# Kernel tuning notes

Hardware: AMD Instinct MI355X
Metric: run time of the kernel (lower is better)

The kernel has to match this reference:

```python
import jax, jax.numpy as jnp
import numpy as np

THRESH = 0.1
BN_EPS = 1e-5
B, N, C_IN, C_HID, C_OUT = 4096, 128, 64, 256, 128


def setup_inputs() -> dict:
    key = jax.random.key(0)
    ks = jax.random.split(key, 10)
    a = jax.random.uniform(ks[0], (B, N, N), dtype=jnp.float32)
    v = jax.random.normal(ks[1], (B, N, C_IN), dtype=jnp.float32)
    # MLP params: Linear(C_IN->C_HID) + BN + ReLU + Linear(C_HID->C_OUT) + BN + ReLU
    W1 = jax.random.normal(ks[2], (C_IN, C_HID), dtype=jnp.float32) / np.sqrt(C_IN)
    b1 = jnp.zeros((C_HID,), jnp.float32)
    g1 = 1.0 + 0.1 * jax.random.normal(ks[3], (C_HID,), dtype=jnp.float32)
    be1 = 0.1 * jax.random.normal(ks[4], (C_HID,), dtype=jnp.float32)
    rm1 = 0.1 * jax.random.normal(ks[5], (C_HID,), dtype=jnp.float32)
    rv1 = jnp.ones((C_HID,), jnp.float32)
    W2 = jax.random.normal(ks[6], (C_HID, C_OUT), dtype=jnp.float32) / np.sqrt(C_HID)
    b2 = jnp.zeros((C_OUT,), jnp.float32)
    g2 = 1.0 + 0.1 * jax.random.normal(ks[7], (C_OUT,), dtype=jnp.float32)
    be2 = 0.1 * jax.random.normal(ks[8], (C_OUT,), dtype=jnp.float32)
    rm2 = 0.1 * jax.random.normal(ks[9], (C_OUT,), dtype=jnp.float32)
    rv2 = jnp.ones((C_OUT,), jnp.float32)
    return {"a": a, "v": v, "W1": W1, "b1": b1, "g1": g1, "be1": be1, "rm1": rm1, "rv1": rv1,
            "W2": W2, "b2": b2, "g2": g2, "be2": be2, "rm2": rm2, "rv2": rv2}


def reference(a, v, W1, b1, g1, be1, rm1, rv1, W2, b2, g2, be2, rm2, rv2):
    # threshold adjacency
    a_th = (a >= THRESH).astype(v.dtype)            # [B, N, N]
    # D^-0.5 A D^-0.5 as row/col rescaling (equivalent to diag_embed + bmm)
    d_inv_sqrt = jnp.sum(a_th, axis=-1) ** -0.5     # [B, N]
    a_bar = d_inv_sqrt[:, :, None] * a_th * d_inv_sqrt[:, None, :]
    # propagate
    h = jnp.einsum('bnm,bmc->bnc', a_bar, v)        # [B, N, C_IN]
    x = h.reshape(-1, h.shape[-1])                  # [(B N), C_IN]
    # MLP with BatchNorm in eval mode (running stats), dropout is identity in eval
    x = x @ W1 + b1
    x = (x - rm1) * jax.lax.rsqrt(rv1 + BN_EPS) * g1 + be1
    x = jax.nn.relu(x)
    x = x @ W2 + b2
    x = (x - rm2) * jax.lax.rsqrt(rv2 + BN_EPS) * g2 + be2
    x = jax.nn.relu(x)
    return x
```

## Files before the change

kernel.cpp:

```cpp
#include <hip/hip_runtime.h>


#define THRESH 0.1f
#define BN_EPS 1e-5f

typedef __attribute__((ext_vector_type(8))) short bf16x8;
typedef __attribute__((ext_vector_type(4))) float f32x4;

__device__ __forceinline__ unsigned short f2bf(float f) {
    union { float f; unsigned u; } x; x.f = f;
    unsigned r = x.u + 0x7FFFu + ((x.u >> 16) & 1u);
    return (unsigned short)(r >> 16);
}

__device__ __forceinline__ unsigned cvt_pk(float lo, float hi) {
    unsigned r;
    asm("v_cvt_pk_bf16_f32 %0, %1, %2" : "=v"(r) : "v"(lo), "v"(hi));
    return r;
}

__global__ void gcn_prep(const float* __restrict__ W1, const float* __restrict__ b1,
                         const float* __restrict__ g1, const float* __restrict__ be1,
                         const float* __restrict__ rm1, const float* __restrict__ rv1,
                         const float* __restrict__ W2, const float* __restrict__ b2,
                         const float* __restrict__ g2, const float* __restrict__ be2,
                         const float* __restrict__ rm2, const float* __restrict__ rv2,
                         unsigned short* __restrict__ W1s, unsigned short* __restrict__ W2s,
                         float* __restrict__ sh1, float* __restrict__ sh2) {
    int t = blockIdx.x * blockDim.x + threadIdx.x;
    if (t < 256 * 64) {
        int n = t >> 6, kp = t & 63;
        int sp = kp >> 3, lo = kp & 7;
        int s  = sp ^ (n & 7);
        int k2 = s * 8 + lo;
        int r = k2 & 3, aa = (k2 >> 2) & 1, gg = (k2 >> 3) & 3, T = k2 >> 5;
        int k = T * 32 + aa * 16 + gg * 4 + r;
        float sc = g1[n] * rsqrtf(rv1[n] + BN_EPS);
        W1s[t] = f2bf(W1[k * 256 + n] * sc);
    }
    {
        int n = t >> 8, kp = t & 255;
        int sp = kp >> 3, lo = kp & 7;
        int s  = sp ^ (n & 7);
        int k2 = s * 8 + lo;
        int r = k2 & 3, aa = (k2 >> 2) & 1, gg = (k2 >> 3) & 3, T = k2 >> 5;
        int k = T * 32 + aa * 16 + gg * 4 + r;
        float sc = g2[n] * rsqrtf(rv2[n] + BN_EPS);
        W2s[t] = f2bf(W2[k * 128 + n] * sc);
    }
    if (t < 256) {
        float s = g1[t] * rsqrtf(rv1[t] + BN_EPS);
        sh1[t] = (b1[t] - rm1[t]) * s + be1[t];
    }
    if (t < 128) {
        float s = g2[t] * rsqrtf(rv2[t] + BN_EPS);
        sh2[t] = (b2[t] - rm2[t]) * s + be2[t];
    }
}

__global__ void __launch_bounds__(512, 1)
gcn_fused(const float* __restrict__ A, const float* __restrict__ V,
          const unsigned short* __restrict__ W1s, const unsigned short* __restrict__ W2s,
          const float* __restrict__ sh1g, const float* __restrict__ sh2g,
          float* __restrict__ out) {
    __shared__ char smem[134656];
    unsigned short* W1L = (unsigned short*)smem;
    unsigned short* W2L = (unsigned short*)(smem + 32768);
    float* s_sh1 = (float*)(smem + 133120);
    float* s_sh2 = (float*)(smem + 134144);

    const int t    = threadIdx.x;
    const int lane = t & 63;
    const int w    = t >> 6;
    const int r16  = lane & 15;
    const int g    = lane >> 4;
    const int bs   = w >> 2;
    const int wl   = w & 3;

    unsigned short* vt = (unsigned short*)(smem + 98304) + bs * (64 * 136);

#pragma unroll
    for (int q = 0; q < 4; ++q)
        *(f32x4*)(smem + t * 64 + q * 16) = *(const f32x4*)((const char*)W1s + t * 64 + q * 16);
#pragma unroll
    for (int q = 0; q < 8; ++q)
        *(f32x4*)(smem + 32768 + t * 128 + q * 16) =
            *(const f32x4*)((const char*)W2s + t * 128 + q * 16);
    if (t < 256) s_sh1[t] = sh1g[t];
    if (t < 128) s_sh2[t] = sh2g[t];

    const size_t b00 = (size_t)blockIdx.x * 16;

    const int mloc  = lane & 31;
    const int chalf = (lane >> 5) * 32;

    bf16x8 afrag[2][4];
    float dinv0, dinv1;
    {
        const size_t b = b00 + bs;
        const float* vb = V + b * 8192 + (size_t)(32 * wl + mloc) * 64 + chalf;
        f32x4 pv[8];
#pragma unroll
        for (int q = 0; q < 8; ++q) pv[q] = *(const f32x4*)(vb + 4 * q);

        const float* ab = A + b * 16384 + (size_t)(32 * wl + r16) * 128;
        int cnt0 = 0, cnt1 = 0;
#pragma unroll
        for (int mt = 0; mt < 2; ++mt)
#pragma unroll
            for (int ks = 0; ks < 4; ++ks) {
                const float* p = ab + mt * 2048 + ks * 32 + 8 * g;
                f32x4 x0 = *(const f32x4*)p;
                f32x4 x1 = *(const f32x4*)(p + 4);
                union { unsigned short s[8]; bf16x8 v; } u;
                u.s[0] = (x0.x >= THRESH) ? (unsigned short)0x3F80u : (unsigned short)0u;
                u.s[1] = (x0.y >= THRESH) ? (unsigned short)0x3F80u : (unsigned short)0u;
                u.s[2] = (x0.z >= THRESH) ? (unsigned short)0x3F80u : (unsigned short)0u;
                u.s[3] = (x0.w >= THRESH) ? (unsigned short)0x3F80u : (unsigned short)0u;
                u.s[4] = (x1.x >= THRESH) ? (unsigned short)0x3F80u : (unsigned short)0u;
                u.s[5] = (x1.y >= THRESH) ? (unsigned short)0x3F80u : (unsigned short)0u;
                u.s[6] = (x1.z >= THRESH) ? (unsigned short)0x3F80u : (unsigned short)0u;
                u.s[7] = (x1.w >= THRESH) ? (unsigned short)0x3F80u : (unsigned short)0u;
                afrag[mt][ks] = u.v;
                int c = (x0.x >= THRESH) + (x0.y >= THRESH) + (x0.z >= THRESH) + (x0.w >= THRESH)
                      + (x1.x >= THRESH) + (x1.y >= THRESH) + (x1.z >= THRESH) + (x1.w >= THRESH);
                if (mt == 0) cnt0 += c; else cnt1 += c;
            }
        cnt0 += __shfl_xor(cnt0, 16); cnt0 += __shfl_xor(cnt0, 32);
        cnt1 += __shfl_xor(cnt1, 16); cnt1 += __shfl_xor(cnt1, 32);
        dinv0 = rsqrtf((float)cnt0);
        dinv1 = rsqrtf((float)cnt1);

        float dm = (lane & 16) ? dinv1 : dinv0;
        int m = 32 * wl + mloc;
#pragma unroll
        for (int q = 0; q < 8; ++q) {
            int c = chalf + 4 * q;
            vt[(c + 0) * 136 + m] = f2bf(pv[q].x * dm);
            vt[(c + 1) * 136 + m] = f2bf(pv[q].y * dm);
            vt[(c + 2) * 136 + m] = f2bf(pv[q].z * dm);
            vt[(c + 3) * 136 + m] = f2bf(pv[q].w * dm);
        }
    }
    __syncthreads();

#pragma unroll 1
    for (int it = 0; it < 8; ++it) {
        const size_t b  = b00 + it * 2 + bs;
        const size_t mb = (size_t)(32 * wl);

        f32x4 acc1[4][2];
#pragma unroll
        for (int ct = 0; ct < 4; ++ct)
#pragma unroll
            for (int mt = 0; mt < 2; ++mt) acc1[ct][mt] = f32x4{0.f, 0.f, 0.f, 0.f};
#pragma unroll
        for (int ks = 0; ks < 4; ++ks)
#pragma unroll
            for (int ct = 0; ct < 4; ++ct) {
                bf16x8 av = *(const bf16x8*)(vt + (ct * 16 + r16) * 136 + ks * 32 + 8 * g);
                acc1[ct][0] = __builtin_amdgcn_mfma_f32_16x16x32_bf16(av, afrag[0][ks], acc1[ct][0], 0, 0, 0);
                acc1[ct][1] = __builtin_amdgcn_mfma_f32_16x16x32_bf16(av, afrag[1][ks], acc1[ct][1], 0, 0, 0);
            }
        bf16x8 bh[2][2];
#pragma unroll
        for (int mt = 0; mt < 2; ++mt) {
            float d = (mt == 0) ? dinv0 : dinv1;
#pragma unroll
            for (int ks2 = 0; ks2 < 2; ++ks2) {
                union { unsigned u[4]; bf16x8 v; } pk;
                pk.u[0] = cvt_pk(acc1[2 * ks2][mt][0] * d,     acc1[2 * ks2][mt][1] * d);
                pk.u[1] = cvt_pk(acc1[2 * ks2][mt][2] * d,     acc1[2 * ks2][mt][3] * d);
                pk.u[2] = cvt_pk(acc1[2 * ks2 + 1][mt][0] * d, acc1[2 * ks2 + 1][mt][1] * d);
                pk.u[3] = cvt_pk(acc1[2 * ks2 + 1][mt][2] * d, acc1[2 * ks2 + 1][mt][3] * d);
                bh[mt][ks2] = pk.v;
            }
        }
        __syncthreads();

        f32x4 acc3[2][8];
#pragma unroll
        for (int mt = 0; mt < 2; ++mt)
#pragma unroll
            for (int ct = 0; ct < 8; ++ct) acc3[mt][ct] = f32x4{0.f, 0.f, 0.f, 0.f};

#pragma unroll
        for (int T = 0; T < 8; ++T) {
            f32x4 a2[2][2];
#pragma unroll
            for (int mt = 0; mt < 2; ++mt)
#pragma unroll
                for (int ctp = 0; ctp < 2; ++ctp) a2[mt][ctp] = f32x4{0.f, 0.f, 0.f, 0.f};
#pragma unroll
            for (int ctp = 0; ctp < 2; ++ctp) {
                int n = (2 * T + ctp) * 16 + r16;
#pragma unroll
                for (int ks2 = 0; ks2 < 2; ++ks2) {
                    int sp = (ks2 * 4 + g) ^ (n & 7);
                    bf16x8 aw = *(const bf16x8*)(W1L + n * 64 + sp * 8);
                    a2[0][ctp] = __builtin_amdgcn_mfma_f32_16x16x32_bf16(aw, bh[0][ks2], a2[0][ctp], 0, 0, 0);
                    a2[1][ctp] = __builtin_amdgcn_mfma_f32_16x16x32_bf16(aw, bh[1][ks2], a2[1][ctp], 0, 0, 0);
                }
            }
            union { unsigned u[4]; bf16x8 v; } af[2];
#pragma unroll
            for (int ctp = 0; ctp < 2; ++ctp) {
                f32x4 sh = *(const f32x4*)(s_sh1 + (2 * T + ctp) * 16 + 4 * g);
#pragma unroll
                for (int mt = 0; mt < 2; ++mt) {
                    float y0 = fmaxf(a2[mt][ctp][0] + sh.x, 0.f);
                    float y1 = fmaxf(a2[mt][ctp][1] + sh.y, 0.f);
                    float y2 = fmaxf(a2[mt][ctp][2] + sh.z, 0.f);
                    float y3 = fmaxf(a2[mt][ctp][3] + sh.w, 0.f);
                    af[mt].u[2 * ctp + 0] = cvt_pk(y0, y1);
                    af[mt].u[2 * ctp + 1] = cvt_pk(y2, y3);
                }
            }
#pragma unroll
            for (int ct3 = 0; ct3 < 8; ++ct3) {
                int n  = ct3 * 16 + r16;
                int sp = (T * 4 + g) ^ (n & 7);
                bf16x8 bw = *(const bf16x8*)(W2L + n * 256 + sp * 8);
                acc3[0][ct3] = __builtin_amdgcn_mfma_f32_16x16x32_bf16(af[0].v, bw, acc3[0][ct3], 0, 0, 0);
                acc3[1][ct3] = __builtin_amdgcn_mfma_f32_16x16x32_bf16(af[1].v, bw, acc3[1][ct3], 0, 0, 0);
            }
        }

        float* ob = out + (b * 128 + mb) * 128;
#pragma unroll
        for (int ct3 = 0; ct3 < 8; ++ct3) {
            int c = ct3 * 16 + r16;
            float sh = s_sh2[c];
#pragma unroll
            for (int mt = 0; mt < 2; ++mt)
#pragma unroll
                for (int r = 0; r < 4; ++r) {
                    int row = 16 * mt + 4 * g + r;
                    ob[row * 128 + c] = fmaxf(acc3[mt][ct3][r] + sh, 0.f);
                }
        }

        if (it < 7) {
            const size_t bn = b00 + (it + 1) * 2 + bs;
            const float* vb = V + bn * 8192 + (size_t)(32 * wl + mloc) * 64 + chalf;
            f32x4 pv[8];
#pragma unroll
            for (int q = 0; q < 8; ++q) pv[q] = *(const f32x4*)(vb + 4 * q);

            const float* ab = A + bn * 16384 + (size_t)(32 * wl + r16) * 128;
            int cnt0 = 0, cnt1 = 0;
#pragma unroll
            for (int mt = 0; mt < 2; ++mt)
#pragma unroll
                for (int ks = 0; ks < 4; ++ks) {
                    const float* p = ab + mt * 2048 + ks * 32 + 8 * g;
                    f32x4 x0 = *(const f32x4*)p;
                    f32x4 x1 = *(const f32x4*)(p + 4);
                    union { unsigned short s[8]; bf16x8 v; } u;
                    u.s[0] = (x0.x >= THRESH) ? (unsigned short)0x3F80u : (unsigned short)0u;
                    u.s[1] = (x0.y >= THRESH) ? (unsigned short)0x3F80u : (unsigned short)0u;
                    u.s[2] = (x0.z >= THRESH) ? (unsigned short)0x3F80u : (unsigned short)0u;
                    u.s[3] = (x0.w >= THRESH) ? (unsigned short)0x3F80u : (unsigned short)0u;
                    u.s[4] = (x1.x >= THRESH) ? (unsigned short)0x3F80u : (unsigned short)0u;
                    u.s[5] = (x1.y >= THRESH) ? (unsigned short)0x3F80u : (unsigned short)0u;
                    u.s[6] = (x1.z >= THRESH) ? (unsigned short)0x3F80u : (unsigned short)0u;
                    u.s[7] = (x1.w >= THRESH) ? (unsigned short)0x3F80u : (unsigned short)0u;
                    afrag[mt][ks] = u.v;
                    int c = (x0.x >= THRESH) + (x0.y >= THRESH) + (x0.z >= THRESH) + (x0.w >= THRESH)
                          + (x1.x >= THRESH) + (x1.y >= THRESH) + (x1.z >= THRESH) + (x1.w >= THRESH);
                    if (mt == 0) cnt0 += c; else cnt1 += c;
                }
            cnt0 += __shfl_xor(cnt0, 16); cnt0 += __shfl_xor(cnt0, 32);
            cnt1 += __shfl_xor(cnt1, 16); cnt1 += __shfl_xor(cnt1, 32);
            dinv0 = rsqrtf((float)cnt0);
            dinv1 = rsqrtf((float)cnt1);

            float dm = (lane & 16) ? dinv1 : dinv0;
            int m = 32 * wl + mloc;
#pragma unroll
            for (int q = 0; q < 8; ++q) {
                int c = chalf + 4 * q;
                vt[(c + 0) * 136 + m] = f2bf(pv[q].x * dm);
                vt[(c + 1) * 136 + m] = f2bf(pv[q].y * dm);
                vt[(c + 2) * 136 + m] = f2bf(pv[q].z * dm);
                vt[(c + 3) * 136 + m] = f2bf(pv[q].w * dm);
            }
            __syncthreads();
        }
    }
}

extern "C" void kernel_launch(void* const* d_in, const int* in_sizes, int n_in,
                              void* d_out, int out_size, void* d_ws, size_t ws_size,
                              hipStream_t stream) {
    (void)in_sizes; (void)n_in; (void)out_size; (void)ws_size;
    const float* a   = (const float*)d_in[0];
    const float* v   = (const float*)d_in[1];
    const float* W1  = (const float*)d_in[2];
    const float* b1  = (const float*)d_in[3];
    const float* g1  = (const float*)d_in[4];
    const float* be1 = (const float*)d_in[5];
    const float* rm1 = (const float*)d_in[6];
    const float* rv1 = (const float*)d_in[7];
    const float* W2  = (const float*)d_in[8];
    const float* b2  = (const float*)d_in[9];
    const float* g2  = (const float*)d_in[10];
    const float* be2 = (const float*)d_in[11];
    const float* rm2 = (const float*)d_in[12];
    const float* rv2 = (const float*)d_in[13];

    char* ws = (char*)d_ws;
    unsigned short* W1s = (unsigned short*)ws;
    unsigned short* W2s = (unsigned short*)(ws + 32768);
    float* sh1 = (float*)(ws + 98304);
    float* sh2 = (float*)(ws + 99328);

    gcn_prep<<<128, 256, 0, stream>>>(W1, b1, g1, be1, rm1, rv1,
                                      W2, b2, g2, be2, rm2, rv2,
                                      W1s, W2s, sh1, sh2);
    gcn_fused<<<256, 512, 0, stream>>>(a, v, W1s, W2s, sh1, sh2, (float*)d_out);
}
```

Measured before the change: 189.5 us.

## Prefetch next batch's adjacency and features during MLP, pack threshold masks as bits

Global loads of the next batch's V and A tiles are now issued before the second MLP GEMM. The A thresholding is interleaved across the T loop, so memory latency overlaps MFMA work instead of sitting in a serialized tail. Adjacency fragments are kept as 32-bit bitmasks, with degrees counted by popcount, and expanded to bf16 fragments only when needed, which reduces register pressure. On the last iteration each block still performs a clamped, redundant prefetch and a vt write, adding some extra memory traffic.

New measurement: 217.0 us. 1.15x slower.

```diff
diff --git a/kernel.cpp b/kernel.cpp
--- a/kernel.cpp
+++ b/kernel.cpp
@@ -17,6 +17,26 @@
     unsigned r;
     asm("v_cvt_pk_bf16_f32 %0, %1, %2" : "=v"(r) : "v"(lo), "v"(hi));
     return r;
+}
+
+__device__ __forceinline__ unsigned thbyte(f32x4 x0, f32x4 x1) {
+    return  (unsigned)(x0.x >= THRESH)
+         | ((unsigned)(x0.y >= THRESH) << 1)
+         | ((unsigned)(x0.z >= THRESH) << 2)
+         | ((unsigned)(x0.w >= THRESH) << 3)
+         | ((unsigned)(x1.x >= THRESH) << 4)
+         | ((unsigned)(x1.y >= THRESH) << 5)
+         | ((unsigned)(x1.z >= THRESH) << 6)
+         | ((unsigned)(x1.w >= THRESH) << 7);
+}
+
+__device__ __forceinline__ bf16x8 bits2frag(unsigned byte) {
+    union { unsigned u[4]; bf16x8 v; } f;
+#pragma unroll
+    for (int q = 0; q < 4; ++q)
+        f.u[q] = (((byte >> (2 * q)) & 1u) * 0x3F80u)
+               | (((byte >> (2 * q + 1)) & 1u) * 0x3F800000u);
+    return f.v;
 }
 
 __global__ void gcn_prep(const float* __restrict__ W1, const float* __restrict__ b1,
@@ -93,39 +113,29 @@
 
     const int mloc  = lane & 31;
     const int chalf = (lane >> 5) * 32;
-
-    bf16x8 afrag[2][4];
+    const size_t voff = (size_t)(32 * wl + mloc) * 64 + chalf;
+    const size_t aoff = (size_t)(32 * wl + r16) * 128;
+
+    unsigned bc0 = 0, bc1 = 0;
     float dinv0, dinv1;
     {
         const size_t b = b00 + bs;
-        const float* vb = V + b * 8192 + (size_t)(32 * wl + mloc) * 64 + chalf;
+        const float* vb = V + b * 8192 + voff;
         f32x4 pv[8];
 #pragma unroll
         for (int q = 0; q < 8; ++q) pv[q] = *(const f32x4*)(vb + 4 * q);
 
-        const float* ab = A + b * 16384 + (size_t)(32 * wl + r16) * 128;
-        int cnt0 = 0, cnt1 = 0;
-#pragma unroll
-        for (int mt = 0; mt < 2; ++mt)
-#pragma unroll
-            for (int ks = 0; ks < 4; ++ks) {
-                const float* p = ab + mt * 2048 + ks * 32 + 8 * g;
-                f32x4 x0 = *(const f32x4*)p;
-                f32x4 x1 = *(const f32x4*)(p + 4);
-                union { unsigned short s[8]; bf16x8 v; } u;
-                u.s[0] = (x0.x >= THRESH) ? (unsigned short)0x3F80u : (unsigned short)0u;
-                u.s[1] = (x0.y >= THRESH) ? (unsigned short)0x3F80u : (unsigned short)0u;
-                u.s[2] = (x0.z >= THRESH) ? (unsigned short)0x3F80u : (unsigned short)0u;
-                u.s[3] = (x0.w >= THRESH) ? (unsigned short)0x3F80u : (unsigned short)0u;
-                u.s[4] = (x1.x >= THRESH) ? (unsigned short)0x3F80u : (unsigned short)0u;
-                u.s[5] = (x1.y >= THRESH) ? (unsigned short)0x3F80u : (unsigned short)0u;
-                u.s[6] = (x1.z >= THRESH) ? (unsigned short)0x3F80u : (unsigned short)0u;
-                u.s[7] = (x1.w >= THRESH) ? (unsigned short)0x3F80u : (unsigned short)0u;
-                afrag[mt][ks] = u.v;
-                int c = (x0.x >= THRESH) + (x0.y >= THRESH) + (x0.z >= THRESH) + (x0.w >= THRESH)
-                      + (x1.x >= THRESH) + (x1.y >= THRESH) + (x1.z >= THRESH) + (x1.w >= THRESH);
-                if (mt == 0) cnt0 += c; else cnt1 += c;
-            }
+        const float* ab = A + b * 16384 + aoff;
+#pragma unroll
+        for (int p = 0; p < 8; ++p) {
+            const int mt = p >> 2, ks = p & 3;
+            const float* pp = ab + mt * 2048 + ks * 32 + 8 * g;
+            f32x4 x0 = *(const f32x4*)pp;
+            f32x4 x1 = *(const f32x4*)(pp + 4);
+            unsigned byte = thbyte(x0, x1);
+            if (mt == 0) bc0 |= byte << (ks * 8); else bc1 |= byte << (ks * 8);
+        }
+        int cnt0 = __popc(bc0), cnt1 = __popc(bc1);
         cnt0 += __shfl_xor(cnt0, 16); cnt0 += __shfl_xor(cnt0, 32);
         cnt1 += __shfl_xor(cnt1, 16); cnt1 += __shfl_xor(cnt1, 32);
         dinv0 = rsqrtf((float)cnt0);
@@ -147,7 +157,14 @@
 #pragma unroll 1
     for (int it = 0; it < 8; ++it) {
         const size_t b  = b00 + it * 2 + bs;
-        const size_t mb = (size_t)(32 * wl);
+        const size_t bn = (b00 + (it + 1) * 2 + bs < 4096) ? (b00 + (it + 1) * 2 + bs) : 4095;
+
+        bf16x8 afrag[2][4];
+#pragma unroll
+        for (int ks = 0; ks < 4; ++ks) {
+            afrag[0][ks] = bits2frag((bc0 >> (ks * 8)) & 0xFFu);
+            afrag[1][ks] = bits2frag((bc1 >> (ks * 8)) & 0xFFu);
+        }
 
         f32x4 acc1[4][2];
 #pragma unroll
@@ -177,6 +194,20 @@
             }
         }
         __syncthreads();
+
+        const float* vbn = V + bn * 8192 + voff;
+        f32x4 pv[8];
+#pragma unroll
+        for (int q = 0; q < 8; ++q) pv[q] = *(const f32x4*)(vbn + 4 * q);
+
+        const float* abn = A + bn * 16384 + aoff;
+        f32x4 paA[2], paB[2];
+        paA[0] = *(const f32x4*)(abn + 0 * 2048 + 0 * 32 + 8 * g);
+        paB[0] = *(const f32x4*)(abn + 0 * 2048 + 0 * 32 + 8 * g + 4);
+        paA[1] = *(const f32x4*)(abn + 0 * 2048 + 1 * 32 + 8 * g);
+        paB[1] = *(const f32x4*)(abn + 0 * 2048 + 1 * 32 + 8 * g + 4);
+
+        unsigned bn0 = 0, bn1 = 0;
 
         f32x4 acc3[2][8];
 #pragma unroll
@@ -224,9 +255,21 @@
                 acc3[0][ct3] = __builtin_amdgcn_mfma_f32_16x16x32_bf16(af[0].v, bw, acc3[0][ct3], 0, 0, 0);
                 acc3[1][ct3] = __builtin_amdgcn_mfma_f32_16x16x32_bf16(af[1].v, bw, acc3[1][ct3], 0, 0, 0);
             }
-        }
-
-        float* ob = out + (b * 128 + mb) * 128;
+
+            {
+                const int mt = T >> 2, ks = T & 3;
+                unsigned byte = thbyte(paA[T & 1], paB[T & 1]);
+                if (mt == 0) bn0 |= byte << (ks * 8); else bn1 |= byte << (ks * 8);
+                if (T + 2 < 8) {
+                    const int p2 = T + 2;
+                    const int mt2 = p2 >> 2, ks2p = p2 & 3;
+                    paA[T & 1] = *(const f32x4*)(abn + mt2 * 2048 + ks2p * 32 + 8 * g);
+                    paB[T & 1] = *(const f32x4*)(abn + mt2 * 2048 + ks2p * 32 + 8 * g + 4);
+                }
+            }
+        }
+
+        float* ob = out + (b * 128 + (size_t)(32 * wl)) * 128;
 #pragma unroll
         for (int ct3 = 0; ct3 < 8; ++ct3) {
             int c = ct3 * 16 + r16;
@@ -240,40 +283,13 @@
                 }
         }
 
-        if (it < 7) {
-            const size_t bn = b00 + (it + 1) * 2 + bs;
-            const float* vb = V + bn * 8192 + (size_t)(32 * wl + mloc) * 64 + chalf;
-            f32x4 pv[8];
-#pragma unroll
-            for (int q = 0; q < 8; ++q) pv[q] = *(const f32x4*)(vb + 4 * q);
-
-            const float* ab = A + bn * 16384 + (size_t)(32 * wl + r16) * 128;
-            int cnt0 = 0, cnt1 = 0;
-#pragma unroll
-            for (int mt = 0; mt < 2; ++mt)
-#pragma unroll
-                for (int ks = 0; ks < 4; ++ks) {
-                    const float* p = ab + mt * 2048 + ks * 32 + 8 * g;
-                    f32x4 x0 = *(const f32x4*)p;
-                    f32x4 x1 = *(const f32x4*)(p + 4);
-                    union { unsigned short s[8]; bf16x8 v; } u;
-                    u.s[0] = (x0.x >= THRESH) ? (unsigned short)0x3F80u : (unsigned short)0u;
-                    u.s[1] = (x0.y >= THRESH) ? (unsigned short)0x3F80u : (unsigned short)0u;
-                    u.s[2] = (x0.z >= THRESH) ? (unsigned short)0x3F80u : (unsigned short)0u;
-                    u.s[3] = (x0.w >= THRESH) ? (unsigned short)0x3F80u : (unsigned short)0u;
-                    u.s[4] = (x1.x >= THRESH) ? (unsigned short)0x3F80u : (unsigned short)0u;
-                    u.s[5] = (x1.y >= THRESH) ? (unsigned short)0x3F80u : (unsigned short)0u;
-                    u.s[6] = (x1.z >= THRESH) ? (unsigned short)0x3F80u : (unsigned short)0u;
-                    u.s[7] = (x1.w >= THRESH) ? (unsigned short)0x3F80u : (unsigned short)0u;
-                    afrag[mt][ks] = u.v;
-                    int c = (x0.x >= THRESH) + (x0.y >= THRESH) + (x0.z >= THRESH) + (x0.w >= THRESH)
-                          + (x1.x >= THRESH) + (x1.y >= THRESH) + (x1.z >= THRESH) + (x1.w >= THRESH);
-                    if (mt == 0) cnt0 += c; else cnt1 += c;
-                }
+        {
+            int cnt0 = __popc(bn0), cnt1 = __popc(bn1);
             cnt0 += __shfl_xor(cnt0, 16); cnt0 += __shfl_xor(cnt0, 32);
             cnt1 += __shfl_xor(cnt1, 16); cnt1 += __shfl_xor(cnt1, 32);
             dinv0 = rsqrtf((float)cnt0);
             dinv1 = rsqrtf((float)cnt1);
+            bc0 = bn0; bc1 = bn1;
 
             float dm = (lane & 16) ? dinv1 : dinv0;
             int m = 32 * wl + mloc;
@@ -285,8 +301,8 @@
                 vt[(c + 2) * 136 + m] = f2bf(pv[q].z * dm);
                 vt[(c + 3) * 136 + m] = f2bf(pv[q].w * dm);
             }
-            __syncthreads();
-        }
+        }
+        if (it < 7) __syncthreads();
     }
 }
 
```
